# Performance work log

Hardware: AMD Instinct MI355X
Metric: run time of the kernel (lower is better)

Reference implementation:

```python
import jax, jax.numpy as jnp
import numpy as np

N, E, G = 30000, 480000, 64
IN, H, L = 24, 512, 6


def setup_inputs() -> dict:
    key = jax.random.key(0)
    ks = jax.random.split(key, 20)
    s = 0.05
    inp = {
        "x": jax.random.normal(ks[0], (N, IN), dtype=jnp.float32),
        "edge_index": jax.random.randint(ks[1], (2, E), 0, N, dtype=jnp.int64),
        "batch": jnp.sort(jax.random.randint(ks[2], (N,), 0, G, dtype=jnp.int64)),
        # node encoder
        "enc_w": jax.random.normal(ks[3], (IN, H), dtype=jnp.float32) * s,
        "enc_b": jnp.zeros((H,), dtype=jnp.float32),
        # per-layer message MLP (stacked over L layers), weights stored [in, out]
        "mlp_w1": jax.random.normal(ks[4], (L, H, H), dtype=jnp.float32) * s,
        "mlp_b1": jnp.zeros((L, H), dtype=jnp.float32),
        "mlp_w2": jax.random.normal(ks[5], (L, H, H), dtype=jnp.float32) * s,
        "mlp_b2": jnp.zeros((L, H), dtype=jnp.float32),
        # per-layer GRUCell params, [in, 3H] layout (gates order: r, z, n)
        "gru_wih": jax.random.normal(ks[6], (L, H, 3 * H), dtype=jnp.float32) * s,
        "gru_whh": jax.random.normal(ks[7], (L, H, 3 * H), dtype=jnp.float32) * s,
        "gru_bih": jnp.zeros((L, 3 * H), dtype=jnp.float32),
        "gru_bhh": jnp.zeros((L, 3 * H), dtype=jnp.float32),
        # head MLP
        "head_w1": jax.random.normal(ks[8], (H, H // 2), dtype=jnp.float32) * s,
        "head_b1": jnp.zeros((H // 2,), dtype=jnp.float32),
        "head_w2": jax.random.normal(ks[9], (H // 2, 1), dtype=jnp.float32) * s,
        "head_b2": jnp.zeros((1,), dtype=jnp.float32),
    }
    return inp


def _forward(x, edge_index, batch, enc_w, enc_b, mlp_w1, mlp_b1, mlp_w2, mlp_b2,
             gru_wih, gru_whh, gru_bih, gru_bhh, head_w1, head_b1, head_w2, head_b2):
    src, dst = edge_index[0], edge_index[1]
    h = x @ enc_w + enc_b  # [N, H]
    for l in range(L):
        # message MLP depends only on x_j, so compute per-node then gather
        msg = jnp.maximum(h @ mlp_w1[l] + mlp_b1[l], 0.0) @ mlp_w2[l] + mlp_b2[l]  # [N, H]
        # scatter-add over edges + self-loop contribution (add_self_loops)
        m = jax.ops.segment_sum(msg[src], dst, num_segments=N) + msg  # [N, H]
        # GRUCell(input=m, hidden=h); torch gate order: reset, update, new
        gi = m @ gru_wih[l] + gru_bih[l]
        gh = h @ gru_whh[l] + gru_bhh[l]
        r = jax.nn.sigmoid(gi[:, :H] + gh[:, :H])
        z = jax.nn.sigmoid(gi[:, H:2 * H] + gh[:, H:2 * H])
        n = jnp.tanh(gi[:, 2 * H:] + r * gh[:, 2 * H:])
        h = (1.0 - z) * n + z * h
    # global mean pool per graph
    sums = jax.ops.segment_sum(h, batch, num_segments=G)
    cnt = jax.ops.segment_sum(jnp.ones((N,), dtype=h.dtype), batch, num_segments=G)
    pooled = sums / jnp.maximum(cnt, 1.0)[:, None]  # [G, H]
    out = jnp.maximum(pooled @ head_w1 + head_b1, 0.0) @ head_w2 + head_b2
    return out[:, 0]  # [G]


def reference(x, edge_index, batch, enc_w, enc_b, mlp_w1, mlp_b1, mlp_w2, mlp_b2,
              gru_wih, gru_whh, gru_bih, gru_bhh, head_w1, head_b1, head_w2, head_b2):
    return _forward(x, edge_index, batch, enc_w, enc_b, mlp_w1, mlp_b1, mlp_w2, mlp_b2,
                    gru_wih, gru_whh, gru_bih, gru_bhh, head_w1, head_b1, head_w2, head_b2)
```

## Files before the change

### kernel.cpp

```cpp
#include <hip/hip_runtime.h>
#include <hip/hip_bf16.h>
#include <math.h>

#define N_NODES 30000
#define N_EDGES 480000
#define N_GRAPH 64
#define DIN 24
#define HD 512
#define NL 6

typedef __hip_bfloat16 bf16;
using short8 = __attribute__((ext_vector_type(8))) short;
using f32x4 = __attribute__((ext_vector_type(4))) float;

#define ASYNC16(gp, lp)                                              \
    __builtin_amdgcn_global_load_lds(                                \
        (const __attribute__((address_space(1))) void*)(gp),         \
        (__attribute__((address_space(3))) void*)(lp), 16, 0, 0)

__device__ __forceinline__ float sigmoidf_(float x) { return 1.0f / (1.0f + expf(-x)); }
__device__ __forceinline__ float b2f(unsigned short u) {
    return __uint_as_float(((unsigned int)u) << 16);
}
__device__ __forceinline__ unsigned short f2b(float f) {
    bf16 b = __float2bfloat16(f);
    return *(unsigned short*)&b;
}

__global__ __launch_bounds__(256) void enc_kernel(const float* __restrict__ x,
                                                  const float* __restrict__ w,
                                                  const float* __restrict__ b,
                                                  bf16* __restrict__ h) {
    __shared__ float xs[DIN];
    int row = blockIdx.x;
    int tid = threadIdx.x;
    if (tid < DIN) xs[tid] = x[row * DIN + tid];
    __syncthreads();
    for (int c = tid; c < HD; c += 256) {
        float acc = b[c];
#pragma unroll
        for (int k = 0; k < DIN; k++) acc = fmaf(xs[k], w[k * HD + c], acc);
        h[(size_t)row * HD + c] = __float2bfloat16(acc);
    }
}

__global__ __launch_bounds__(256) void twcvt_kernel(const float* __restrict__ W,
                                                    bf16* __restrict__ WtH,
                                                    bf16* __restrict__ WtL, int Nc) {
    __shared__ float s[32][33];
    int l = blockIdx.z;
    const float* Wp = W + (size_t)l * HD * Nc;
    size_t ob = (size_t)l * HD * Nc;
    int k0 = blockIdx.y * 32, c0 = blockIdx.x * 32;
    int tx = threadIdx.x & 31, ty = threadIdx.x >> 5;
    for (int r = ty; r < 32; r += 8) s[r][tx] = Wp[(size_t)(k0 + r) * Nc + c0 + tx];
    __syncthreads();
    for (int r = ty; r < 32; r += 8) {
        float v = s[tx][r];
        unsigned short hu = f2b(v);
        float hf = b2f(hu);
        size_t o = ob + (size_t)(c0 + r) * HD + k0 + tx;
        *(unsigned short*)&WtH[o] = hu;
        WtL[o] = __float2bfloat16(v - hf);
    }
}

template <bool RELU>
__global__ __launch_bounds__(256) void gemm_mfma(const bf16* __restrict__ A,
                                                 const bf16* __restrict__ WtH,
                                                 const bf16* __restrict__ WtL,
                                                 const float* __restrict__ bias,
                                                 bf16* __restrict__ C, int n) {
    __shared__ bf16 As[128 * 32];
    __shared__ bf16 BH[128 * 32];
    __shared__ bf16 BL[128 * 32];
    int tid = threadIdx.x;
    int wv = tid >> 6, lane = tid & 63;
    int quad = lane >> 4, l16 = lane & 15;
    int crow = lane >> 2, cseg = lane & 3;
    int gseg = cseg ^ ((crow >> 1) & 3);
    int fsw = (quad ^ ((l16 >> 1) & 3)) * 8;
    int row0 = blockIdx.y * 128, col0 = blockIdx.x * 128;
    f32x4 acc[2][8] = {};

    int aoff[4], alds[4];
    int boff[8];
    const bf16* wb = (wv == 2) ? WtH : WtL;
    bf16* bdst = (wv == 2) ? BH : BL;
    if (wv < 2) {
#pragma unroll
        for (int j = 0; j < 4; j++) {
            int ch = wv * 4 + j;
            int gr = row0 + ch * 16 + crow;
            if (gr > n - 1) gr = n - 1;
            aoff[j] = gr * HD + gseg * 8;
            alds[j] = ch * 512;
        }
    } else {
#pragma unroll
        for (int s = 0; s < 8; s++) boff[s] = (col0 + s * 16 + crow) * HD + gseg * 8;
    }

    for (int kt = 0; kt < 512; kt += 32) {
        if (wv < 2) {
#pragma unroll
            for (int j = 0; j < 4; j++) ASYNC16(&A[aoff[j] + kt], &As[alds[j]]);
        } else {
#pragma unroll
            for (int s = 0; s < 8; s++) ASYNC16(&wb[boff[s] + kt], &bdst[s * 512]);
        }
        __syncthreads();
        short8 af[2];
#pragma unroll
        for (int i = 0; i < 2; i++)
            af[i] = *(const short8*)&As[(wv * 32 + i * 16 + l16) * 32 + fsw];
#pragma unroll
        for (int t = 0; t < 8; t++) {
            int fo = (t * 16 + l16) * 32 + fsw;
            short8 bh = *(const short8*)&BH[fo];
            short8 bl = *(const short8*)&BL[fo];
#pragma unroll
            for (int i = 0; i < 2; i++) {
                acc[i][t] = __builtin_amdgcn_mfma_f32_16x16x32_bf16(af[i], bh, acc[i][t], 0, 0, 0);
                acc[i][t] = __builtin_amdgcn_mfma_f32_16x16x32_bf16(af[i], bl, acc[i][t], 0, 0, 0);
            }
        }
        __syncthreads();
    }
#pragma unroll
    for (int t = 0; t < 8; t++) {
        int col = col0 + t * 16 + l16;
        float bb = bias[col];
#pragma unroll
        for (int i = 0; i < 2; i++) {
#pragma unroll
            for (int r = 0; r < 4; r++) {
                int row = row0 + wv * 32 + i * 16 + quad * 4 + r;
                if (row < n) {
                    float v = acc[i][t][r] + bb;
                    if (RELU) v = fmaxf(v, 0.0f);
                    C[(size_t)row * HD + col] = __float2bfloat16(v);
                }
            }
        }
    }
}

__global__ __launch_bounds__(256, 2) void gru_mfma(const bf16* __restrict__ M,
                                                   const bf16* __restrict__ Hc,
                                                   const bf16* __restrict__ WiH,
                                                   const bf16* __restrict__ WiL,
                                                   const bf16* __restrict__ WhH,
                                                   const bf16* __restrict__ WhL,
                                                   const float* __restrict__ bih,
                                                   const float* __restrict__ bhh,
                                                   bf16* __restrict__ Hn, int n) {
    __shared__ bf16 Ms[128 * 32];
    __shared__ bf16 Hs[128 * 32];
    __shared__ bf16 Ws[12 * 64 * 32];
    int tid = threadIdx.x;
    int wv = tid >> 6, lane = tid & 63;
    int quad = lane >> 4, l16 = lane & 15;
    int crow = lane >> 2, cseg = lane & 3;
    int gseg = cseg ^ ((crow >> 1) & 3);
    int fsw = (quad ^ ((l16 >> 1) & 3)) * 8;
    int row0 = blockIdx.y * 128, col0 = blockIdx.x * 64;
    f32x4 aR[2][4] = {}, aZ[2][4] = {}, aI[2][4] = {}, aHn[2][4] = {};

    int moff[8];
    const bf16* wgp[4];
    int wlds[4];
    if (wv == 0) {
#pragma unroll
        for (int j = 0; j < 8; j++) {
            int gr = row0 + j * 16 + crow;
            if (gr > n - 1) gr = n - 1;
            moff[j] = gr * HD + gseg * 8;
        }
    } else {
        const bf16* wbase[4] = {WiH, WiL, WhH, WhL};
#pragma unroll
        for (int pp = 0; pp < 4; pp++) {
            int p = (wv - 1) * 4 + pp;
            int mat = (p >= 6);
            int q = p - mat * 6;
            int g = q >> 1, pl = q & 1;
            const bf16* base = wbase[mat * 2 + pl] + (size_t)(g * HD + col0) * HD;
            wgp[pp] = base + crow * HD + gseg * 8;
            wlds[pp] = p * 2048;
        }
    }

    for (int kt = 0; kt < 512; kt += 32) {
        if (wv == 0) {
#pragma unroll
            for (int j = 0; j < 8; j++) {
                ASYNC16(&M[moff[j] + kt], &Ms[j * 512]);
                ASYNC16(&Hc[moff[j] + kt], &Hs[j * 512]);
            }
        } else {
#pragma unroll
            for (int pp = 0; pp < 4; pp++)
#pragma unroll
                for (int s = 0; s < 4; s++)
                    ASYNC16(wgp[pp] + (size_t)s * 16 * HD + kt, &Ws[wlds[pp] + s * 512]);
        }
        __syncthreads();
        short8 am[2], ah[2];
#pragma unroll
        for (int i = 0; i < 2; i++) {
            am[i] = *(const short8*)&Ms[(wv * 32 + i * 16 + l16) * 32 + fsw];
            ah[i] = *(const short8*)&Hs[(wv * 32 + i * 16 + l16) * 32 + fsw];
        }
#pragma unroll
        for (int t = 0; t < 4; t++) {
            int fo = (t * 16 + l16) * 32 + fsw;
            short8 wrh = *(const short8*)&Ws[0 * 2048 + fo];
            short8 wrl = *(const short8*)&Ws[1 * 2048 + fo];
            short8 wzh = *(const short8*)&Ws[2 * 2048 + fo];
            short8 wzl = *(const short8*)&Ws[3 * 2048 + fo];
            short8 wnh = *(const short8*)&Ws[4 * 2048 + fo];
            short8 wnl = *(const short8*)&Ws[5 * 2048 + fo];
            short8 vrh = *(const short8*)&Ws[6 * 2048 + fo];
            short8 vrl = *(const short8*)&Ws[7 * 2048 + fo];
            short8 vzh = *(const short8*)&Ws[8 * 2048 + fo];
            short8 vzl = *(const short8*)&Ws[9 * 2048 + fo];
            short8 vnh = *(const short8*)&Ws[10 * 2048 + fo];
            short8 vnl = *(const short8*)&Ws[11 * 2048 + fo];
#pragma unroll
            for (int i = 0; i < 2; i++) {
                aR[i][t] = __builtin_amdgcn_mfma_f32_16x16x32_bf16(am[i], wrh, aR[i][t], 0, 0, 0);
                aR[i][t] = __builtin_amdgcn_mfma_f32_16x16x32_bf16(am[i], wrl, aR[i][t], 0, 0, 0);
                aR[i][t] = __builtin_amdgcn_mfma_f32_16x16x32_bf16(ah[i], vrh, aR[i][t], 0, 0, 0);
                aR[i][t] = __builtin_amdgcn_mfma_f32_16x16x32_bf16(ah[i], vrl, aR[i][t], 0, 0, 0);
                aZ[i][t] = __builtin_amdgcn_mfma_f32_16x16x32_bf16(am[i], wzh, aZ[i][t], 0, 0, 0);
                aZ[i][t] = __builtin_amdgcn_mfma_f32_16x16x32_bf16(am[i], wzl, aZ[i][t], 0, 0, 0);
                aZ[i][t] = __builtin_amdgcn_mfma_f32_16x16x32_bf16(ah[i], vzh, aZ[i][t], 0, 0, 0);
                aZ[i][t] = __builtin_amdgcn_mfma_f32_16x16x32_bf16(ah[i], vzl, aZ[i][t], 0, 0, 0);
                aI[i][t] = __builtin_amdgcn_mfma_f32_16x16x32_bf16(am[i], wnh, aI[i][t], 0, 0, 0);
                aI[i][t] = __builtin_amdgcn_mfma_f32_16x16x32_bf16(am[i], wnl, aI[i][t], 0, 0, 0);
                aHn[i][t] = __builtin_amdgcn_mfma_f32_16x16x32_bf16(ah[i], vnh, aHn[i][t], 0, 0, 0);
                aHn[i][t] = __builtin_amdgcn_mfma_f32_16x16x32_bf16(ah[i], vnl, aHn[i][t], 0, 0, 0);
            }
        }
        __syncthreads();
    }
    const unsigned short* hp = (const unsigned short*)Hc;
#pragma unroll
    for (int t = 0; t < 4; t++) {
        int col = col0 + t * 16 + l16;
        float brz = bih[col] + bhh[col];
        float bzz = bih[HD + col] + bhh[HD + col];
        float bin_ = bih[2 * HD + col];
        float bhn_ = bhh[2 * HD + col];
#pragma unroll
        for (int i = 0; i < 2; i++) {
#pragma unroll
            for (int r = 0; r < 4; r++) {
                int row = row0 + wv * 32 + i * 16 + quad * 4 + r;
                if (row < n) {
                    float rg = sigmoidf_(aR[i][t][r] + brz);
                    float zg = sigmoidf_(aZ[i][t][r] + bzz);
                    float ng = tanhf(aI[i][t][r] + bin_ + rg * (aHn[i][t][r] + bhn_));
                    float hold = b2f(hp[(size_t)row * HD + col]);
                    Hn[(size_t)row * HD + col] = __float2bfloat16((1.0f - zg) * ng + zg * hold);
                }
            }
        }
    }
}

__global__ __launch_bounds__(256) void deg_kernel(const int* __restrict__ dst,
                                                  int* __restrict__ deg) {
    int e = blockIdx.x * 256 + threadIdx.x;
    if (e < N_EDGES) atomicAdd(&deg[dst[e]], 1);
}

__global__ __launch_bounds__(1024) void scan_kernel(const int* __restrict__ deg,
                                                    int* __restrict__ offs) {
    __shared__ int buf[1024];
    __shared__ int carry_s;
    int tid = threadIdx.x;
    if (tid == 0) carry_s = 0;
    __syncthreads();
    for (int base = 0; base < N_NODES; base += 1024) {
        int v = (base + tid < N_NODES) ? deg[base + tid] : 0;
        buf[tid] = v;
        __syncthreads();
        for (int s = 1; s < 1024; s <<= 1) {
            int t = (tid >= s) ? buf[tid - s] : 0;
            __syncthreads();
            buf[tid] += t;
            __syncthreads();
        }
        int incl = buf[tid];
        if (base + tid < N_NODES) offs[base + tid] = carry_s + incl - v;
        __syncthreads();
        if (tid == 0) carry_s += buf[1023];
        __syncthreads();
    }
    if (tid == 0) offs[N_NODES] = carry_s;
}

__global__ __launch_bounds__(256) void bucket_kernel(const int* __restrict__ src,
                                                     const int* __restrict__ dst,
                                                     const int* __restrict__ offs,
                                                     int* __restrict__ cursor,
                                                     unsigned short* __restrict__ elist) {
    int e = blockIdx.x * 256 + threadIdx.x;
    if (e >= N_EDGES) return;
    int d = dst[e];
    int pos = atomicAdd(&cursor[d], 1);
    elist[offs[d] + pos] = (unsigned short)src[e];
}

__global__ __launch_bounds__(256) void gather_kernel(const bf16* __restrict__ msg,
                                                     bf16* __restrict__ m,
                                                     const unsigned short* __restrict__ elist,
                                                     const int* __restrict__ offs) {
    int nid = blockIdx.x, tid = threadIdx.x;
    int beg = offs[nid], end = offs[nid + 1];
    const unsigned int* mp = (const unsigned int*)msg;
    unsigned int u = mp[(size_t)nid * 256 + tid];
    float ax = b2f((unsigned short)(u & 0xffffu));
    float ay = b2f((unsigned short)(u >> 16));
    int e = beg;
    for (; e + 3 < end; e += 4) {
        unsigned int v0 = mp[(size_t)elist[e] * 256 + tid];
        unsigned int v1 = mp[(size_t)elist[e + 1] * 256 + tid];
        unsigned int v2 = mp[(size_t)elist[e + 2] * 256 + tid];
        unsigned int v3 = mp[(size_t)elist[e + 3] * 256 + tid];
        ax += b2f((unsigned short)(v0 & 0xffffu)) + b2f((unsigned short)(v1 & 0xffffu)) +
              b2f((unsigned short)(v2 & 0xffffu)) + b2f((unsigned short)(v3 & 0xffffu));
        ay += b2f((unsigned short)(v0 >> 16)) + b2f((unsigned short)(v1 >> 16)) +
              b2f((unsigned short)(v2 >> 16)) + b2f((unsigned short)(v3 >> 16));
    }
    for (; e < end; e++) {
        unsigned int v0 = mp[(size_t)elist[e] * 256 + tid];
        ax += b2f((unsigned short)(v0 & 0xffffu));
        ay += b2f((unsigned short)(v0 >> 16));
    }
    unsigned int out = ((unsigned int)f2b(ay) << 16) | (unsigned int)f2b(ax);
    ((unsigned int*)m)[(size_t)nid * 256 + tid] = out;
}

__global__ __launch_bounds__(256) void pool_kernel(const bf16* __restrict__ h,
                                                   const int* __restrict__ batch,
                                                   float* __restrict__ pooled,
                                                   float* __restrict__ cnt) {
    int g = blockIdx.x;
    int col = blockIdx.y * 256 + threadIdx.x;
    int lo = 0, hi = N_NODES;
    while (lo < hi) { int mid = (lo + hi) >> 1; if (batch[mid] < g) lo = mid + 1; else hi = mid; }
    int gs = lo;
    hi = N_NODES;
    while (lo < hi) { int mid = (lo + hi) >> 1; if (batch[mid] < g + 1) lo = mid + 1; else hi = mid; }
    int ge = lo;
    const unsigned short* hp = (const unsigned short*)h;
    float acc = 0.0f;
    int r = gs;
    for (; r + 3 < ge; r += 4) {
        acc += b2f(hp[(size_t)r * HD + col]) + b2f(hp[(size_t)(r + 1) * HD + col]) +
               b2f(hp[(size_t)(r + 2) * HD + col]) + b2f(hp[(size_t)(r + 3) * HD + col]);
    }
    for (; r < ge; r++) acc += b2f(hp[(size_t)r * HD + col]);
    pooled[g * HD + col] = acc;
    if (blockIdx.y == 0 && threadIdx.x == 0) cnt[g] = (float)(ge - gs);
}

__global__ __launch_bounds__(256) void head_kernel(const float* __restrict__ pooled,
                                                   const float* __restrict__ cnt,
                                                   const float* __restrict__ w1,
                                                   const float* __restrict__ b1,
                                                   const float* __restrict__ w2,
                                                   const float* __restrict__ b2,
                                                   float* __restrict__ out) {
    __shared__ float prow[HD];
    __shared__ float red[256];
    int g = blockIdx.x, tid = threadIdx.x;
    float c = fmaxf(cnt[g], 1.0f);
    for (int j = tid; j < HD; j += 256) prow[j] = pooled[g * HD + j] / c;
    __syncthreads();
    float acc = b1[tid];
    for (int k = 0; k < HD; k++) acc = fmaf(prow[k], w1[k * 256 + tid], acc);
    red[tid] = fmaxf(acc, 0.0f) * w2[tid];
    __syncthreads();
    for (int s = 128; s > 0; s >>= 1) {
        if (tid < s) red[tid] += red[tid + s];
        __syncthreads();
    }
    if (tid == 0) out[g] = red[0] + b2[0];
}

extern "C" void kernel_launch(void* const* d_in, const int* in_sizes, int n_in,
                              void* d_out, int out_size, void* d_ws, size_t ws_size,
                              hipStream_t stream) {
    const float* x = (const float*)d_in[0];
    const int* eidx = (const int*)d_in[1];
    const int* batch = (const int*)d_in[2];
    const float* enc_w = (const float*)d_in[3];
    const float* enc_b = (const float*)d_in[4];
    const float* mlp_w1 = (const float*)d_in[5];
    const float* mlp_b1 = (const float*)d_in[6];
    const float* mlp_w2 = (const float*)d_in[7];
    const float* mlp_b2 = (const float*)d_in[8];
    const float* gru_wih = (const float*)d_in[9];
    const float* gru_whh = (const float*)d_in[10];
    const float* gru_bih = (const float*)d_in[11];
    const float* gru_bhh = (const float*)d_in[12];
    const float* head_w1 = (const float*)d_in[13];
    const float* head_b1 = (const float*)d_in[14];
    const float* head_w2 = (const float*)d_in[15];
    const float* head_b2 = (const float*)d_in[16];
    const int* src = eidx;
    const int* dst = eidx + N_EDGES;

    const size_t NH = (size_t)N_NODES * HD;
    char* p = (char*)d_ws;
    auto alloc = [&](size_t bytes) { char* q = p; p += (bytes + 255) & ~(size_t)255; return q; };
    bf16* S0 = (bf16*)alloc(NH * 2);
    bf16* S1 = (bf16*)alloc(NH * 2);
    bf16* S2 = (bf16*)alloc(NH * 2);
    bf16* w1tH = (bf16*)alloc((size_t)NL * HD * HD * 2);
    bf16* w1tL = (bf16*)alloc((size_t)NL * HD * HD * 2);
    bf16* w2tH = (bf16*)alloc((size_t)NL * HD * HD * 2);
    bf16* w2tL = (bf16*)alloc((size_t)NL * HD * HD * 2);
    bf16* wihtH = (bf16*)alloc((size_t)NL * 3 * HD * HD * 2);
    bf16* wihtL = (bf16*)alloc((size_t)NL * 3 * HD * HD * 2);
    bf16* whhtH = (bf16*)alloc((size_t)NL * 3 * HD * HD * 2);
    bf16* whhtL = (bf16*)alloc((size_t)NL * 3 * HD * HD * 2);
    float* pooled = (float*)alloc((size_t)N_GRAPH * HD * 4);
    float* cnt = (float*)alloc(N_GRAPH * 4);
    int* deg = (int*)alloc((N_NODES + 1) * 4);
    int* offs = (int*)alloc((N_NODES + 1) * 4);
    unsigned short* elist = (unsigned short*)alloc((size_t)N_EDGES * 2);

    twcvt_kernel<<<dim3(16, 16, NL), 256, 0, stream>>>(mlp_w1, w1tH, w1tL, HD);
    twcvt_kernel<<<dim3(16, 16, NL), 256, 0, stream>>>(mlp_w2, w2tH, w2tL, HD);
    twcvt_kernel<<<dim3(48, 16, NL), 256, 0, stream>>>(gru_wih, wihtH, wihtL, 3 * HD);
    twcvt_kernel<<<dim3(48, 16, NL), 256, 0, stream>>>(gru_whh, whhtH, whhtL, 3 * HD);

    hipMemsetAsync(deg, 0, (N_NODES + 1) * sizeof(int), stream);
    deg_kernel<<<(N_EDGES + 255) / 256, 256, 0, stream>>>(dst, deg);
    scan_kernel<<<1, 1024, 0, stream>>>(deg, offs);
    hipMemsetAsync(deg, 0, (N_NODES + 1) * sizeof(int), stream);
    bucket_kernel<<<(N_EDGES + 255) / 256, 256, 0, stream>>>(src, dst, offs, deg, elist);

    enc_kernel<<<N_NODES, 256, 0, stream>>>(x, enc_w, enc_b, S0);

    bf16* hcur = S0;
    bf16* hoth = S1;
    dim3 ggrid(4, (N_NODES + 127) / 128);
    dim3 ugrid(8, (N_NODES + 127) / 128);

    for (int l = 0; l < NL; l++) {
        size_t wsq = (size_t)l * HD * HD;
        size_t wgq = (size_t)l * 3 * HD * HD;
        const float* b1 = mlp_b1 + (size_t)l * HD;
        const float* b2 = mlp_b2 + (size_t)l * HD;
        const float* bih = gru_bih + (size_t)l * 3 * HD;
        const float* bhh = gru_bhh + (size_t)l * 3 * HD;

        gemm_mfma<true><<<ggrid, 256, 0, stream>>>(hcur, w1tH + wsq, w1tL + wsq, b1, hoth, N_NODES);
        gemm_mfma<false><<<ggrid, 256, 0, stream>>>(hoth, w2tH + wsq, w2tL + wsq, b2, S2, N_NODES);
        gather_kernel<<<N_NODES, 256, 0, stream>>>(S2, hoth, elist, offs);
        gru_mfma<<<ugrid, 256, 0, stream>>>(hoth, hcur, wihtH + wgq, wihtL + wgq,
                                            whhtH + wgq, whhtL + wgq, bih, bhh, S2, N_NODES);
        bf16* newh = S2;
        S2 = hcur;
        hcur = newh;
    }

    pool_kernel<<<dim3(N_GRAPH, 2), 256, 0, stream>>>(hcur, batch, pooled, cnt);
    head_kernel<<<N_GRAPH, 256, 0, stream>>>(pooled, cnt, head_w1, head_b1, head_w2, head_b2,
                                             (float*)d_out);
}
```

Measured before the change: 2.856 ms.

## Reassign warp tiles to split columns instead of rows in GEMM and GRU kernels

Changes the per-wave work split in the MLP GEMM and GRU kernels so that each wave owns a column slice across all 128 rows, rather than a 32-row slice across all columns. The weight fragments are now loaded from LDS once per k-step and held in registers, while activation fragments are streamed per row tile. This reduces LDS reads of the larger, doubled hi/lo weight tiles. In exchange, every wave now reads all A/M/H rows, and the epilogue stores have a different access pattern.

```diff
diff --git a/kernel.cpp b/kernel.cpp
--- a/kernel.cpp
+++ b/kernel.cpp
@@ -110,34 +110,35 @@
             for (int s = 0; s < 8; s++) ASYNC16(&wb[boff[s] + kt], &bdst[s * 512]);
         }
         __syncthreads();
-        short8 af[2];
-#pragma unroll
-        for (int i = 0; i < 2; i++)
-            af[i] = *(const short8*)&As[(wv * 32 + i * 16 + l16) * 32 + fsw];
-#pragma unroll
-        for (int t = 0; t < 8; t++) {
-            int fo = (t * 16 + l16) * 32 + fsw;
-            short8 bh = *(const short8*)&BH[fo];
-            short8 bl = *(const short8*)&BL[fo];
-#pragma unroll
-            for (int i = 0; i < 2; i++) {
-                acc[i][t] = __builtin_amdgcn_mfma_f32_16x16x32_bf16(af[i], bh, acc[i][t], 0, 0, 0);
-                acc[i][t] = __builtin_amdgcn_mfma_f32_16x16x32_bf16(af[i], bl, acc[i][t], 0, 0, 0);
+        short8 bfr[2][2];
+#pragma unroll
+        for (int t = 0; t < 2; t++) {
+            int fo = ((wv * 2 + t) * 16 + l16) * 32 + fsw;
+            bfr[t][0] = *(const short8*)&BH[fo];
+            bfr[t][1] = *(const short8*)&BL[fo];
+        }
+#pragma unroll
+        for (int i = 0; i < 8; i++) {
+            short8 af = *(const short8*)&As[(i * 16 + l16) * 32 + fsw];
+#pragma unroll
+            for (int t = 0; t < 2; t++) {
+                acc[t][i] = __builtin_amdgcn_mfma_f32_16x16x32_bf16(af, bfr[t][0], acc[t][i], 0, 0, 0);
+                acc[t][i] = __builtin_amdgcn_mfma_f32_16x16x32_bf16(af, bfr[t][1], acc[t][i], 0, 0, 0);
             }
         }
         __syncthreads();
     }
 #pragma unroll
-    for (int t = 0; t < 8; t++) {
-        int col = col0 + t * 16 + l16;
+    for (int t = 0; t < 2; t++) {
+        int col = col0 + (wv * 2 + t) * 16 + l16;
         float bb = bias[col];
 #pragma unroll
-        for (int i = 0; i < 2; i++) {
+        for (int i = 0; i < 8; i++) {
 #pragma unroll
             for (int r = 0; r < 4; r++) {
-                int row = row0 + wv * 32 + i * 16 + quad * 4 + r;
+                int row = row0 + i * 16 + quad * 4 + r;
                 if (row < n) {
-                    float v = acc[i][t][r] + bb;
+                    float v = acc[t][i][r] + bb;
                     if (RELU) v = fmaxf(v, 0.0f);
                     C[(size_t)row * HD + col] = __float2bfloat16(v);
                 }
@@ -165,7 +166,7 @@
     int gseg = cseg ^ ((crow >> 1) & 3);
     int fsw = (quad ^ ((l16 >> 1) & 3)) * 8;
     int row0 = blockIdx.y * 128, col0 = blockIdx.x * 64;
-    f32x4 aR[2][4] = {}, aZ[2][4] = {}, aI[2][4] = {}, aHn[2][4] = {};
+    f32x4 aR[8] = {}, aZ[8] = {}, aI[8] = {}, aHn[8] = {};
 
     int moff[8];
     const bf16* wgp[4];
@@ -206,65 +207,55 @@
                     ASYNC16(wgp[pp] + (size_t)s * 16 * HD + kt, &Ws[wlds[pp] + s * 512]);
         }
         __syncthreads();
-        short8 am[2], ah[2];
-#pragma unroll
-        for (int i = 0; i < 2; i++) {
-            am[i] = *(const short8*)&Ms[(wv * 32 + i * 16 + l16) * 32 + fsw];
-            ah[i] = *(const short8*)&Hs[(wv * 32 + i * 16 + l16) * 32 + fsw];
-        }
-#pragma unroll
-        for (int t = 0; t < 4; t++) {
-            int fo = (t * 16 + l16) * 32 + fsw;
-            short8 wrh = *(const short8*)&Ws[0 * 2048 + fo];
-            short8 wrl = *(const short8*)&Ws[1 * 2048 + fo];
-            short8 wzh = *(const short8*)&Ws[2 * 2048 + fo];
-            short8 wzl = *(const short8*)&Ws[3 * 2048 + fo];
-            short8 wnh = *(const short8*)&Ws[4 * 2048 + fo];
-            short8 wnl = *(const short8*)&Ws[5 * 2048 + fo];
-            short8 vrh = *(const short8*)&Ws[6 * 2048 + fo];
-            short8 vrl = *(const short8*)&Ws[7 * 2048 + fo];
-            short8 vzh = *(const short8*)&Ws[8 * 2048 + fo];
-            short8 vzl = *(const short8*)&Ws[9 * 2048 + fo];
-            short8 vnh = *(const short8*)&Ws[10 * 2048 + fo];
-            short8 vnl = *(const short8*)&Ws[11 * 2048 + fo];
-#pragma unroll
-            for (int i = 0; i < 2; i++) {
-                aR[i][t] = __builtin_amdgcn_mfma_f32_16x16x32_bf16(am[i], wrh, aR[i][t], 0, 0, 0);
-                aR[i][t] = __builtin_amdgcn_mfma_f32_16x16x32_bf16(am[i], wrl, aR[i][t], 0, 0, 0);
-                aR[i][t] = __builtin_amdgcn_mfma_f32_16x16x32_bf16(ah[i], vrh, aR[i][t], 0, 0, 0);
-                aR[i][t] = __builtin_amdgcn_mfma_f32_16x16x32_bf16(ah[i], vrl, aR[i][t], 0, 0, 0);
-                aZ[i][t] = __builtin_amdgcn_mfma_f32_16x16x32_bf16(am[i], wzh, aZ[i][t], 0, 0, 0);
-                aZ[i][t] = __builtin_amdgcn_mfma_f32_16x16x32_bf16(am[i], wzl, aZ[i][t], 0, 0, 0);
-                aZ[i][t] = __builtin_amdgcn_mfma_f32_16x16x32_bf16(ah[i], vzh, aZ[i][t], 0, 0, 0);
-                aZ[i][t] = __builtin_amdgcn_mfma_f32_16x16x32_bf16(ah[i], vzl, aZ[i][t], 0, 0, 0);
-                aI[i][t] = __builtin_amdgcn_mfma_f32_16x16x32_bf16(am[i], wnh, aI[i][t], 0, 0, 0);
-                aI[i][t] = __builtin_amdgcn_mfma_f32_16x16x32_bf16(am[i], wnl, aI[i][t], 0, 0, 0);
-                aHn[i][t] = __builtin_amdgcn_mfma_f32_16x16x32_bf16(ah[i], vnh, aHn[i][t], 0, 0, 0);
-                aHn[i][t] = __builtin_amdgcn_mfma_f32_16x16x32_bf16(ah[i], vnl, aHn[i][t], 0, 0, 0);
-            }
+        int fo = (wv * 16 + l16) * 32 + fsw;
+        short8 wrh = *(const short8*)&Ws[0 * 2048 + fo];
+        short8 wrl = *(const short8*)&Ws[1 * 2048 + fo];
+        short8 wzh = *(const short8*)&Ws[2 * 2048 + fo];
+        short8 wzl = *(const short8*)&Ws[3 * 2048 + fo];
+        short8 wnh = *(const short8*)&Ws[4 * 2048 + fo];
+        short8 wnl = *(const short8*)&Ws[5 * 2048 + fo];
+        short8 vrh = *(const short8*)&Ws[6 * 2048 + fo];
+        short8 vrl = *(const short8*)&Ws[7 * 2048 + fo];
+        short8 vzh = *(const short8*)&Ws[8 * 2048 + fo];
+        short8 vzl = *(const short8*)&Ws[9 * 2048 + fo];
+        short8 vnh = *(const short8*)&Ws[10 * 2048 + fo];
+        short8 vnl = *(const short8*)&Ws[11 * 2048 + fo];
+#pragma unroll
+        for (int i = 0; i < 8; i++) {
+            short8 am = *(const short8*)&Ms[(i * 16 + l16) * 32 + fsw];
+            short8 ah = *(const short8*)&Hs[(i * 16 + l16) * 32 + fsw];
+            aR[i] = __builtin_amdgcn_mfma_f32_16x16x32_bf16(am, wrh, aR[i], 0, 0, 0);
+            aR[i] = __builtin_amdgcn_mfma_f32_16x16x32_bf16(am, wrl, aR[i], 0, 0, 0);
+            aR[i] = __builtin_amdgcn_mfma_f32_16x16x32_bf16(ah, vrh, aR[i], 0, 0, 0);
+            aR[i] = __builtin_amdgcn_mfma_f32_16x16x32_bf16(ah, vrl, aR[i], 0, 0, 0);
+            aZ[i] = __builtin_amdgcn_mfma_f32_16x16x32_bf16(am, wzh, aZ[i], 0, 0, 0);
+            aZ[i] = __builtin_amdgcn_mfma_f32_16x16x32_bf16(am, wzl, aZ[i], 0, 0, 0);
+            aZ[i] = __builtin_amdgcn_mfma_f32_16x16x32_bf16(ah, vzh, aZ[i], 0, 0, 0);
+            aZ[i] = __builtin_amdgcn_mfma_f32_16x16x32_bf16(ah, vzl, aZ[i], 0, 0, 0);
+            aI[i] = __builtin_amdgcn_mfma_f32_16x16x32_bf16(am, wnh, aI[i], 0, 0, 0);
+            aI[i] = __builtin_amdgcn_mfma_f32_16x16x32_bf16(am, wnl, aI[i], 0, 0, 0);
+            aHn[i] = __builtin_amdgcn_mfma_f32_16x16x32_bf16(ah, vnh, aHn[i], 0, 0, 0);
+            aHn[i] = __builtin_amdgcn_mfma_f32_16x16x32_bf16(ah, vnl, aHn[i], 0, 0, 0);
         }
         __syncthreads();
     }
     const unsigned short* hp = (const unsigned short*)Hc;
-#pragma unroll
-    for (int t = 0; t < 4; t++) {
-        int col = col0 + t * 16 + l16;
-        float brz = bih[col] + bhh[col];
-        float bzz = bih[HD + col] + bhh[HD + col];
-        float bin_ = bih[2 * HD + col];
-        float bhn_ = bhh[2 * HD + col];
-#pragma unroll
-        for (int i = 0; i < 2; i++) {
-#pragma unroll
-            for (int r = 0; r < 4; r++) {
-                int row = row0 + wv * 32 + i * 16 + quad * 4 + r;
-                if (row < n) {
-                    float rg = sigmoidf_(aR[i][t][r] + brz);
-                    float zg = sigmoidf_(aZ[i][t][r] + bzz);
-                    float ng = tanhf(aI[i][t][r] + bin_ + rg * (aHn[i][t][r] + bhn_));
-                    float hold = b2f(hp[(size_t)row * HD + col]);
-                    Hn[(size_t)row * HD + col] = __float2bfloat16((1.0f - zg) * ng + zg * hold);
-                }
+    int col = col0 + wv * 16 + l16;
+    float brz = bih[col] + bhh[col];
+    float bzz = bih[HD + col] + bhh[HD + col];
+    float bin_ = bih[2 * HD + col];
+    float bhn_ = bhh[2 * HD + col];
+#pragma unroll
+    for (int i = 0; i < 8; i++) {
+#pragma unroll
+        for (int r = 0; r < 4; r++) {
+            int row = row0 + i * 16 + quad * 4 + r;
+            if (row < n) {
+                float rg = sigmoidf_(aR[i][r] + brz);
+                float zg = sigmoidf_(aZ[i][r] + bzz);
+                float ng = tanhf(aI[i][r] + bin_ + rg * (aHn[i][r] + bhn_));
+                float hold = b2f(hp[(size_t)row * HD + col]);
+                Hn[(size_t)row * HD + col] = __float2bfloat16((1.0f - zg) * ng + zg * hold);
             }
         }
     }
```

Measured after the change: 2.854 ms. Within noise of the previous version (-0.1%).
